# Optimization experiments

Hardware: AMD Instinct MI355X
Metric: run time of the kernel (lower is better)

## Reference

```python
import jax, jax.numpy as jnp
import numpy as np
import math

B, S, D = 1, 2048, 512
H = 8
DH = D // H
WIN = 128  # window_size
EPS = 1e-5


def _layernorm(x, g, b):
    mu = jnp.mean(x, axis=-1, keepdims=True)
    var = jnp.mean((x - mu) ** 2, axis=-1, keepdims=True)
    return (x - mu) * jax.lax.rsqrt(var + EPS) * g + b


def _local_attention(q, k, v, window_size):
    # q,k,v: [B,H,S,DH]. Faithful to F.pad + unfold: zero-padded keys
    # participate in softmax with score 0 (no masking), as in the original.
    w = window_size // 2
    W = 2 * w + 1
    kp = jnp.pad(k, ((0, 0), (0, 0), (w, w), (0, 0)))
    vp = jnp.pad(v, ((0, 0), (0, 0), (w, w), (0, 0)))
    idx = jnp.arange(q.shape[2])[:, None] + jnp.arange(W)[None, :]  # [S,W]
    k_win = kp[:, :, idx]  # [B,H,S,W,DH]
    v_win = vp[:, :, idx]  # [B,H,S,W,DH]
    scores = jnp.einsum('bhsd,bhswd->bhsw', q, k_win) / math.sqrt(q.shape[-1])
    attn = jax.nn.softmax(scores, axis=-1)
    return jnp.einsum('bhsw,bhswd->bhsd', attn, v_win)


def setup_inputs() -> dict:
    key = jax.random.key(0)
    ks = jax.random.split(key, 8)
    sc = 0.02
    return {
        'x': jax.random.normal(ks[0], (B, S, D), dtype=jnp.float32),
        'w_qkv': jax.random.normal(ks[1], (D, 3 * D), dtype=jnp.float32) * sc,
        'b_qkv': jnp.zeros((3 * D,), dtype=jnp.float32),
        'w_out': jax.random.normal(ks[2], (D, D), dtype=jnp.float32) * sc,
        'b_out': jnp.zeros((D,), dtype=jnp.float32),
        'ln_g': jnp.ones((D,), dtype=jnp.float32),
        'ln_b': jnp.zeros((D,), dtype=jnp.float32),
        'w1': jax.random.normal(ks[3], (D, 4 * D), dtype=jnp.float32) * sc,
        'b1': jnp.zeros((4 * D,), dtype=jnp.float32),
        'w2': jax.random.normal(ks[4], (4 * D, D), dtype=jnp.float32) * sc,
        'b2': jnp.zeros((D,), dtype=jnp.float32),
    }


def reference(x, w_qkv, b_qkv, w_out, b_out, ln_g, ln_b, w1, b1, w2, b2):
    residual = x
    xn = _layernorm(x, ln_g, ln_b)
    qkv = xn @ w_qkv + b_qkv                       # [B,S,3D]
    qkv = qkv.reshape(B, S, 3, H, DH)
    qkv = jnp.transpose(qkv, (2, 0, 3, 1, 4))      # [3,B,H,S,DH]
    q, k, v = qkv[0], qkv[1], qkv[2]
    attn_out = _local_attention(q, k, v, WIN)       # [B,H,S,DH]
    attn_out = jnp.transpose(attn_out, (0, 2, 1, 3)).reshape(B, S, D)
    attn_out = attn_out @ w_out + b_out
    out = residual + attn_out
    # FFN applied directly to `out` (no second norm in original)
    ffn = jax.nn.gelu(out @ w1 + b1, approximate=False) @ w2 + b2
    return out + ffn
```

## Files before the change

### kernel.cpp

```cpp
#include <hip/hip_runtime.h>
#include <math.h>

#define S_LEN 2048
#define DMODEL 512
#define NHEAD 8
#define DHEAD 64
#define LN_EPS 1e-5f

typedef __bf16 bf16;
typedef __bf16 bf16x8 __attribute__((ext_vector_type(8)));
typedef __bf16 bf16x2 __attribute__((ext_vector_type(2)));
typedef float f32x4 __attribute__((ext_vector_type(4)));

__device__ __forceinline__ float wave_reduce_sum(float x) {
#pragma unroll
  for (int off = 32; off > 0; off >>= 1) x += __shfl_xor(x, off);
  return x;
}

__global__ __launch_bounds__(256) void ln_kernel(const float* __restrict__ x,
                                                 const float* __restrict__ g,
                                                 const float* __restrict__ b,
                                                 bf16* __restrict__ xn) {
  const int row = blockIdx.x;
  const int tid = threadIdx.x;
  const float2 v = ((const float2*)(x + (size_t)row * DMODEL))[tid];
  float s = v.x + v.y;
  float s2 = v.x * v.x + v.y * v.y;
  s = wave_reduce_sum(s);
  s2 = wave_reduce_sum(s2);
  __shared__ float red[2][4];
  const int wv = tid >> 6, ln = tid & 63;
  if (ln == 0) { red[0][wv] = s; red[1][wv] = s2; }
  __syncthreads();
  s = red[0][0] + red[0][1] + red[0][2] + red[0][3];
  s2 = red[1][0] + red[1][1] + red[1][2] + red[1][3];
  const float mu = s * (1.0f / DMODEL);
  const float var = s2 * (1.0f / DMODEL) - mu * mu;
  const float rs = rsqrtf(var + LN_EPS);
  const float2 gg = ((const float2*)g)[tid];
  const float2 bb = ((const float2*)b)[tid];
  bf16x2 o;
  o[0] = (bf16)((v.x - mu) * rs * gg.x + bb.x);
  o[1] = (bf16)((v.y - mu) * rs * gg.y + bb.y);
  ((bf16x2*)(xn + (size_t)row * DMODEL))[tid] = o;
}

__global__ __launch_bounds__(256) void transpose_all(
    const float* __restrict__ w_qkv, const float* __restrict__ w_out,
    const float* __restrict__ w1, const float* __restrict__ w2,
    bf16* __restrict__ wqkvT, bf16* __restrict__ woutT,
    bf16* __restrict__ w1T, bf16* __restrict__ w2T) {
  int b = blockIdx.x;
  const float* W; bf16* WT; int K, N, bx, by;
  if (b < 768)       { W = w_qkv; WT = wqkvT; K = 512;  N = 1536; bx = b % 48; by = b / 48; }
  else if (b < 1024) { b -= 768;  W = w_out; WT = woutT; K = 512;  N = 512;  bx = b % 16; by = b / 16; }
  else if (b < 2048) { b -= 1024; W = w1;    WT = w1T;   K = 512;  N = 2048; bx = b % 64; by = b / 64; }
  else               { b -= 2048; W = w2;    WT = w2T;   K = 2048; N = 512;  bx = b % 16; by = b / 16; }
  __shared__ float t[32][33];
  const int c = threadIdx.x & 31, r8 = threadIdx.x >> 5;
  const int n0 = bx * 32, k0 = by * 32;
#pragma unroll
  for (int it = 0; it < 4; it++) {
    const int r = r8 + it * 8;
    t[r][c] = W[(size_t)(k0 + r) * N + n0 + c];
  }
  __syncthreads();
#pragma unroll
  for (int it = 0; it < 4; it++) {
    const int r = r8 + it * 8;
    WT[(size_t)(n0 + r) * K + k0 + c] = (bf16)t[c][r];
  }
}

__global__ __launch_bounds__(256) void v_transpose(const bf16* __restrict__ qkvb,
                                                   bf16* __restrict__ vT) {
  __shared__ bf16 t[32][33];
  const int c = threadIdx.x & 31, r8 = threadIdx.x >> 5;
  const int c0 = blockIdx.x * 32;
  const int s0 = blockIdx.y * 32;
#pragma unroll
  for (int it = 0; it < 4; it++) {
    const int r = r8 + it * 8;
    t[r][c] = qkvb[(size_t)(s0 + r) * 1536 + 1024 + c0 + c];
  }
  __syncthreads();
#pragma unroll
  for (int it = 0; it < 4; it++) {
    const int r = r8 + it * 8;
    vT[(size_t)(c0 + r) * S_LEN + s0 + c] = t[c][r];
  }
}

template <int MODE>
__device__ __forceinline__ void epilogue_store(float v, const float* res,
                                               float* Cf, bf16* Cb,
                                               size_t row, size_t col, int N) {
  if (MODE == 2) v = 0.5f * v * (1.0f + erff(v * 0.70710678118654752f));
  if (MODE == 1 || MODE == 3) v += res[row * N + col];
  if (MODE == 1 || MODE == 3) Cf[row * N + col] = v;
  if (MODE == 0 || MODE == 1 || MODE == 2) Cb[row * N + col] = (bf16)v;
}

template <int MODE>
__global__ __launch_bounds__(256) void mmA_kernel(const bf16* __restrict__ A,
                                                  const bf16* __restrict__ BT,
                                                  const float* __restrict__ bias,
                                                  const float* __restrict__ res,
                                                  float* __restrict__ Cf,
                                                  bf16* __restrict__ Cb,
                                                  int N, int K) {
  __shared__ bf16 As[2][64 * 64];
  __shared__ bf16 Bs[2][128 * 64];
  const int tid = threadIdx.x;
  const int wave = tid >> 6, lane = tid & 63;
  const int lr = lane & 15, kg = lane >> 4;
  const int rowBase = blockIdx.y * 64, colBase = blockIdx.x * 128;

  f32x4 acc[4][2] = {};
  const int niter = K >> 6;

  auto stage = [&](int kk, int buf) {
#pragma unroll
    for (int r = 0; r < 2; ++r) {
      const int c = wave * 2 + r;
      const int elem = c * 512 + lane * 8;
      const int s = elem >> 11, row = (elem >> 5) & 63, kp = elem & 31;
      const bf16* ga = A + (size_t)(rowBase + row) * K + kk + s * 32 + kp;
      __builtin_amdgcn_global_load_lds(
          (const __attribute__((address_space(1))) void*)ga,
          (__attribute__((address_space(3))) void*)(&As[buf][c * 512]), 16, 0, 0);
    }
#pragma unroll
    for (int r = 0; r < 4; ++r) {
      const int c = wave * 4 + r;
      const int elem = c * 512 + lane * 8;
      const int s = elem >> 12, row = (elem >> 5) & 127, kp = elem & 31;
      const bf16* gb = BT + (size_t)(colBase + row) * K + kk + s * 32 + kp;
      __builtin_amdgcn_global_load_lds(
          (const __attribute__((address_space(1))) void*)gb,
          (__attribute__((address_space(3))) void*)(&Bs[buf][c * 512]), 16, 0, 0);
    }
  };

  stage(0, 0);
  for (int it = 0; it < niter; ++it) {
    const int cur = it & 1;
    __syncthreads();
    if (it + 1 < niter) stage((it + 1) << 6, cur ^ 1);
    const bf16* as = As[cur];
    const bf16* bs = Bs[cur];
#pragma unroll
    for (int s = 0; s < 2; ++s) {
      bf16x8 af[4], bfr[2];
#pragma unroll
      for (int i = 0; i < 4; ++i)
        af[i] = *(const bf16x8*)(as + s * 2048 + (i * 16 + lr) * 32 + kg * 8);
#pragma unroll
      for (int j = 0; j < 2; ++j)
        bfr[j] = *(const bf16x8*)(bs + s * 4096 + (wave * 32 + j * 16 + lr) * 32 + kg * 8);
#pragma unroll
      for (int i = 0; i < 4; ++i)
#pragma unroll
        for (int j = 0; j < 2; ++j)
          acc[i][j] = __builtin_amdgcn_mfma_f32_16x16x32_bf16(af[i], bfr[j],
                                                              acc[i][j], 0, 0, 0);
    }
  }

#pragma unroll
  for (int j = 0; j < 2; ++j) {
    const int col = colBase + wave * 32 + j * 16 + lr;
    const float bs = bias[col];
#pragma unroll
    for (int i = 0; i < 4; ++i)
#pragma unroll
      for (int r = 0; r < 4; ++r)
        epilogue_store<MODE>(acc[i][j][r] + bs, res, Cf, Cb,
                             (size_t)(rowBase + i * 16 + kg * 4 + r),
                             (size_t)col, N);
  }
}

template <int MODE>
__global__ __launch_bounds__(256) void mmB_kernel(const bf16* __restrict__ A,
                                                  const bf16* __restrict__ BT,
                                                  const float* __restrict__ bias,
                                                  const float* __restrict__ res,
                                                  float* __restrict__ Cf,
                                                  bf16* __restrict__ Cb,
                                                  int N, int K) {
  __shared__ bf16 As[2][32 * 64];
  __shared__ bf16 Bs[2][64 * 64];
  const int tid = threadIdx.x;
  const int wave = tid >> 6, lane = tid & 63;
  const int lr = lane & 15, kg = lane >> 4;
  const int rowBase = blockIdx.y * 32, colBase = blockIdx.x * 64;

  f32x4 acc[2] = {};
  const int niter = K >> 6;

  auto stage = [&](int kk, int buf) {
    {
      const int c = wave;
      const int elem = c * 512 + lane * 8;
      const int s = elem >> 10, row = (elem >> 5) & 31, kp = elem & 31;
      const bf16* ga = A + (size_t)(rowBase + row) * K + kk + s * 32 + kp;
      __builtin_amdgcn_global_load_lds(
          (const __attribute__((address_space(1))) void*)ga,
          (__attribute__((address_space(3))) void*)(&As[buf][c * 512]), 16, 0, 0);
    }
#pragma unroll
    for (int r = 0; r < 2; ++r) {
      const int c = wave * 2 + r;
      const int elem = c * 512 + lane * 8;
      const int s = elem >> 11, row = (elem >> 5) & 63, kp = elem & 31;
      const bf16* gb = BT + (size_t)(colBase + row) * K + kk + s * 32 + kp;
      __builtin_amdgcn_global_load_lds(
          (const __attribute__((address_space(1))) void*)gb,
          (__attribute__((address_space(3))) void*)(&Bs[buf][c * 512]), 16, 0, 0);
    }
  };

  stage(0, 0);
  for (int it = 0; it < niter; ++it) {
    const int cur = it & 1;
    __syncthreads();
    if (it + 1 < niter) stage((it + 1) << 6, cur ^ 1);
    const bf16* as = As[cur];
    const bf16* bs = Bs[cur];
#pragma unroll
    for (int s = 0; s < 2; ++s) {
      bf16x8 af[2], bfr;
#pragma unroll
      for (int i = 0; i < 2; ++i)
        af[i] = *(const bf16x8*)(as + s * 1024 + (i * 16 + lr) * 32 + kg * 8);
      bfr = *(const bf16x8*)(bs + s * 2048 + (wave * 16 + lr) * 32 + kg * 8);
#pragma unroll
      for (int i = 0; i < 2; ++i)
        acc[i] = __builtin_amdgcn_mfma_f32_16x16x32_bf16(af[i], bfr, acc[i], 0, 0, 0);
    }
  }

  {
    const int col = colBase + wave * 16 + lr;
    const float bs = bias[col];
#pragma unroll
    for (int i = 0; i < 2; ++i)
#pragma unroll
      for (int r = 0; r < 4; ++r)
        epilogue_store<MODE>(acc[i][r] + bs, res, Cf, Cb,
                             (size_t)(rowBase + i * 16 + kg * 4 + r),
                             (size_t)col, N);
  }
}

__global__ __launch_bounds__(256) void attn_fused(const bf16* __restrict__ qkvb,
                                                  const bf16* __restrict__ vT,
                                                  bf16* __restrict__ attnb) {
  __shared__ bf16 Kl[192][72];
  __shared__ bf16 Vt[64][200];
  __shared__ bf16 Ql[64][72];

  const int tid = threadIdx.x;
  const int s0 = blockIdx.x * 64;
  const int hc = blockIdx.y * DHEAD;

  {
    const int row = tid >> 2, c0 = (tid & 3) * 16;
    const bf16* src = qkvb + (size_t)(s0 + row) * 1536 + hc + c0;
    *(bf16x8*)&Ql[row][c0] = *(const bf16x8*)src;
    *(bf16x8*)&Ql[row][c0 + 8] = *(const bf16x8*)(src + 8);
  }
#pragma unroll
  for (int it = 0; it < 3; it++) {
    const int row = it * 64 + (tid >> 2), c0 = (tid & 3) * 16;
    const int p = s0 - 64 + row;
    bf16x8 a, b;
    if (p >= 0 && p < S_LEN) {
      const bf16* src = qkvb + (size_t)p * 1536 + 512 + hc + c0;
      a = *(const bf16x8*)src;
      b = *(const bf16x8*)(src + 8);
    } else {
#pragma unroll
      for (int j = 0; j < 8; j++) { a[j] = (bf16)0.f; b[j] = (bf16)0.f; }
    }
    *(bf16x8*)&Kl[row][c0] = a;
    *(bf16x8*)&Kl[row][c0 + 8] = b;
  }
  {
    const int d = tid >> 2, r0 = (tid & 3) * 48;
    const bf16* src = vT + (size_t)(hc + d) * S_LEN;
#pragma unroll
    for (int i = 0; i < 6; i++) {
      const int p0 = s0 - 64 + r0 + i * 8;
      bf16x8 v;
      if (p0 >= 0 && p0 + 8 <= S_LEN) {
        v = *(const bf16x8*)(src + p0);
      } else {
#pragma unroll
        for (int j = 0; j < 8; j++) {
          const int p = p0 + j;
          v[j] = (p >= 0 && p < S_LEN) ? src[p] : (bf16)0.f;
        }
      }
      *(bf16x8*)&Vt[d][r0 + i * 8] = v;
    }
  }
  __syncthreads();

  const int wv = tid >> 6, lane = tid & 63;
  const int lr = lane & 15, kg = lane >> 4;

  f32x4 c[12] = {};
#pragma unroll
  for (int step = 0; step < 2; step++) {
    const bf16x8 qf = *(const bf16x8*)&Ql[wv * 16 + lr][step * 32 + kg * 8];
#pragma unroll
    for (int t = 0; t < 12; t++) {
      const bf16x8 kf = *(const bf16x8*)&Kl[t * 16 + lr][step * 32 + kg * 8];
      c[t] = __builtin_amdgcn_mfma_f32_16x16x32_bf16(qf, kf, c[t], 0, 0, 0);
    }
  }

  float e[12][4];
  float inv[4];
#pragma unroll
  for (int rr = 0; rr < 4; rr++) {
    const int q = wv * 16 + kg * 4 + rr;
    float m = -1e30f;
#pragma unroll
    for (int t = 0; t < 12; t++) {
      const int col = t * 16 + lr;
      if (col >= q && col <= q + 128) m = fmaxf(m, c[t][rr] * 0.125f);
    }
#pragma unroll
    for (int off = 1; off < 16; off <<= 1) m = fmaxf(m, __shfl_xor(m, off));
    float sum = 0.f;
#pragma unroll
    for (int t = 0; t < 12; t++) {
      const int col = t * 16 + lr;
      const bool valid = (col >= q) && (col <= q + 128);
      const float ev = valid ? __expf(c[t][rr] * 0.125f - m) : 0.f;
      e[t][rr] = ev;
      sum += ev;
    }
#pragma unroll
    for (int off = 1; off < 16; off <<= 1) sum += __shfl_xor(sum, off);
    inv[rr] = 1.f / sum;
  }

  __syncthreads();

  bf16* Pl = (bf16*)Kl + wv * (16 * 200);
#pragma unroll
  for (int rr = 0; rr < 4; rr++)
#pragma unroll
    for (int t = 0; t < 12; t++)
      Pl[(kg * 4 + rr) * 200 + t * 16 + lr] = (bf16)(e[t][rr] * inv[rr]);

  f32x4 o[4] = {};
#pragma unroll
  for (int step = 0; step < 6; step++) {
    const bf16x8 pf = *(const bf16x8*)&Pl[lr * 200 + step * 32 + kg * 8];
#pragma unroll
    for (int jt = 0; jt < 4; jt++) {
      const bf16x8 vf = *(const bf16x8*)&Vt[jt * 16 + lr][step * 32 + kg * 8];
      o[jt] = __builtin_amdgcn_mfma_f32_16x16x32_bf16(pf, vf, o[jt], 0, 0, 0);
    }
  }

#pragma unroll
  for (int jt = 0; jt < 4; jt++)
#pragma unroll
    for (int rr = 0; rr < 4; rr++) {
      const int q = wv * 16 + kg * 4 + rr;
      attnb[(size_t)(s0 + q) * DMODEL + hc + jt * 16 + lr] = (bf16)o[jt][rr];
    }
}

extern "C" void kernel_launch(void* const* d_in, const int* in_sizes, int n_in,
                              void* d_out, int out_size, void* d_ws, size_t ws_size,
                              hipStream_t stream) {
  const float* x     = (const float*)d_in[0];
  const float* w_qkv = (const float*)d_in[1];
  const float* b_qkv = (const float*)d_in[2];
  const float* w_out = (const float*)d_in[3];
  const float* b_out = (const float*)d_in[4];
  const float* ln_g  = (const float*)d_in[5];
  const float* ln_b  = (const float*)d_in[6];
  const float* w1    = (const float*)d_in[7];
  const float* b1    = (const float*)d_in[8];
  const float* w2    = (const float*)d_in[9];
  const float* b2    = (const float*)d_in[10];
  float* out = (float*)d_out;

  char* w = (char*)d_ws;
  const size_t MB = 1u << 20;
  bf16* xn    = (bf16*)(w + 0);
  bf16* attnb = (bf16*)(w + 0);
  bf16* qkvb  = (bf16*)(w + 2 * MB);
  bf16* outb  = (bf16*)(w + 2 * MB);
  bf16* vT    = (bf16*)(w + 8 * MB);
  bf16* h1    = (bf16*)(w + 10 * MB);
  bf16* wqkvT = (bf16*)(w + 18 * MB);
  bf16* woutT = (bf16*)(w + 19 * MB + 512 * 1024);
  bf16* w1T   = (bf16*)(w + 20 * MB);
  bf16* w2T   = (bf16*)(w + 22 * MB);

  transpose_all<<<3072, 256, 0, stream>>>(w_qkv, w_out, w1, w2,
                                          wqkvT, woutT, w1T, w2T);
  ln_kernel<<<S_LEN, 256, 0, stream>>>(x, ln_g, ln_b, xn);
  mmA_kernel<0><<<dim3(12, 32), 256, 0, stream>>>(xn, wqkvT, b_qkv, nullptr,
                                                  nullptr, qkvb, 1536, 512);
  v_transpose<<<dim3(16, 64), 256, 0, stream>>>(qkvb, vT);
  attn_fused<<<dim3(32, 8), 256, 0, stream>>>(qkvb, vT, attnb);
  mmB_kernel<1><<<dim3(8, 64), 256, 0, stream>>>(attnb, woutT, b_out, x, out,
                                                 outb, 512, 512);
  mmA_kernel<2><<<dim3(16, 32), 256, 0, stream>>>(outb, w1T, b1, nullptr,
                                                  nullptr, h1, 2048, 512);
  mmB_kernel<3><<<dim3(8, 64), 256, 0, stream>>>(h1, w2T, b2, out, out,
                                                 nullptr, 512, 2048);
}
```

Measured before the change: 147.7 us.

## Fuse LN with weight transpose, write V transposed from QKV GEMM, shrink GEMM tiles

Merges layernorm and weight transposition into a single prep launch. The QKV GEMM epilogue now writes the V columns directly in transposed layout, which removes the separate v_transpose kernel. The large GEMM tile goes from 64x128 to 64x64 with a 2x2 wave arrangement, doubling the grid for the QKV and FFN1 GEMMs. Staging addresses are precomputed outside the K loop. The aim is fewer launches and better occupancy, at the cost of less reuse per tile and strided bf16x4 stores into vT.

```diff
diff --git a/kernel.cpp b/kernel.cpp
--- a/kernel.cpp
+++ b/kernel.cpp
@@ -9,6 +9,7 @@
 
 typedef __bf16 bf16;
 typedef __bf16 bf16x8 __attribute__((ext_vector_type(8)));
+typedef __bf16 bf16x4 __attribute__((ext_vector_type(4)));
 typedef __bf16 bf16x2 __attribute__((ext_vector_type(2)));
 typedef float f32x4 __attribute__((ext_vector_type(4)));
 
@@ -18,47 +19,46 @@
   return x;
 }
 
-__global__ __launch_bounds__(256) void ln_kernel(const float* __restrict__ x,
-                                                 const float* __restrict__ g,
-                                                 const float* __restrict__ b,
-                                                 bf16* __restrict__ xn) {
-  const int row = blockIdx.x;
-  const int tid = threadIdx.x;
-  const float2 v = ((const float2*)(x + (size_t)row * DMODEL))[tid];
-  float s = v.x + v.y;
-  float s2 = v.x * v.x + v.y * v.y;
-  s = wave_reduce_sum(s);
-  s2 = wave_reduce_sum(s2);
-  __shared__ float red[2][4];
-  const int wv = tid >> 6, ln = tid & 63;
-  if (ln == 0) { red[0][wv] = s; red[1][wv] = s2; }
-  __syncthreads();
-  s = red[0][0] + red[0][1] + red[0][2] + red[0][3];
-  s2 = red[1][0] + red[1][1] + red[1][2] + red[1][3];
-  const float mu = s * (1.0f / DMODEL);
-  const float var = s2 * (1.0f / DMODEL) - mu * mu;
-  const float rs = rsqrtf(var + LN_EPS);
-  const float2 gg = ((const float2*)g)[tid];
-  const float2 bb = ((const float2*)b)[tid];
-  bf16x2 o;
-  o[0] = (bf16)((v.x - mu) * rs * gg.x + bb.x);
-  o[1] = (bf16)((v.y - mu) * rs * gg.y + bb.y);
-  ((bf16x2*)(xn + (size_t)row * DMODEL))[tid] = o;
-}
-
-__global__ __launch_bounds__(256) void transpose_all(
-    const float* __restrict__ w_qkv, const float* __restrict__ w_out,
-    const float* __restrict__ w1, const float* __restrict__ w2,
+__global__ __launch_bounds__(256) void prep_kernel(
+    const float* __restrict__ x, const float* __restrict__ ln_g,
+    const float* __restrict__ ln_b, const float* __restrict__ w_qkv,
+    const float* __restrict__ w_out, const float* __restrict__ w1,
+    const float* __restrict__ w2, bf16* __restrict__ xn,
     bf16* __restrict__ wqkvT, bf16* __restrict__ woutT,
     bf16* __restrict__ w1T, bf16* __restrict__ w2T) {
+  __shared__ float t[32][33];
   int b = blockIdx.x;
+  const int tid = threadIdx.x;
+  if (b < 2048) {
+    const float2 v = ((const float2*)(x + (size_t)b * DMODEL))[tid];
+    float s = v.x + v.y;
+    float s2 = v.x * v.x + v.y * v.y;
+    s = wave_reduce_sum(s);
+    s2 = wave_reduce_sum(s2);
+    __shared__ float red[2][4];
+    const int wv = tid >> 6, ln = tid & 63;
+    if (ln == 0) { red[0][wv] = s; red[1][wv] = s2; }
+    __syncthreads();
+    s = red[0][0] + red[0][1] + red[0][2] + red[0][3];
+    s2 = red[1][0] + red[1][1] + red[1][2] + red[1][3];
+    const float mu = s * (1.0f / DMODEL);
+    const float var = s2 * (1.0f / DMODEL) - mu * mu;
+    const float rs = rsqrtf(var + LN_EPS);
+    const float2 gg = ((const float2*)ln_g)[tid];
+    const float2 bb = ((const float2*)ln_b)[tid];
+    bf16x2 o;
+    o[0] = (bf16)((v.x - mu) * rs * gg.x + bb.x);
+    o[1] = (bf16)((v.y - mu) * rs * gg.y + bb.y);
+    ((bf16x2*)(xn + (size_t)b * DMODEL))[tid] = o;
+    return;
+  }
+  b -= 2048;
   const float* W; bf16* WT; int K, N, bx, by;
   if (b < 768)       { W = w_qkv; WT = wqkvT; K = 512;  N = 1536; bx = b % 48; by = b / 48; }
   else if (b < 1024) { b -= 768;  W = w_out; WT = woutT; K = 512;  N = 512;  bx = b % 16; by = b / 16; }
   else if (b < 2048) { b -= 1024; W = w1;    WT = w1T;   K = 512;  N = 2048; bx = b % 64; by = b / 64; }
   else               { b -= 2048; W = w2;    WT = w2T;   K = 2048; N = 512;  bx = b % 16; by = b / 16; }
-  __shared__ float t[32][33];
-  const int c = threadIdx.x & 31, r8 = threadIdx.x >> 5;
+  const int c = tid & 31, r8 = tid >> 5;
   const int n0 = bx * 32, k0 = by * 32;
 #pragma unroll
   for (int it = 0; it < 4; it++) {
@@ -70,25 +70,6 @@
   for (int it = 0; it < 4; it++) {
     const int r = r8 + it * 8;
     WT[(size_t)(n0 + r) * K + k0 + c] = (bf16)t[c][r];
-  }
-}
-
-__global__ __launch_bounds__(256) void v_transpose(const bf16* __restrict__ qkvb,
-                                                   bf16* __restrict__ vT) {
-  __shared__ bf16 t[32][33];
-  const int c = threadIdx.x & 31, r8 = threadIdx.x >> 5;
-  const int c0 = blockIdx.x * 32;
-  const int s0 = blockIdx.y * 32;
-#pragma unroll
-  for (int it = 0; it < 4; it++) {
-    const int r = r8 + it * 8;
-    t[r][c] = qkvb[(size_t)(s0 + r) * 1536 + 1024 + c0 + c];
-  }
-  __syncthreads();
-#pragma unroll
-  for (int it = 0; it < 4; it++) {
-    const int r = r8 + it * 8;
-    vT[(size_t)(c0 + r) * S_LEN + s0 + c] = t[c][r];
   }
 }
 
@@ -99,49 +80,50 @@
   if (MODE == 2) v = 0.5f * v * (1.0f + erff(v * 0.70710678118654752f));
   if (MODE == 1 || MODE == 3) v += res[row * N + col];
   if (MODE == 1 || MODE == 3) Cf[row * N + col] = v;
-  if (MODE == 0 || MODE == 1 || MODE == 2) Cb[row * N + col] = (bf16)v;
+  if (MODE == 1 || MODE == 2) Cb[row * N + col] = (bf16)v;
 }
 
 template <int MODE>
-__global__ __launch_bounds__(256) void mmA_kernel(const bf16* __restrict__ A,
+__global__ __launch_bounds__(256) void mmC_kernel(const bf16* __restrict__ A,
                                                   const bf16* __restrict__ BT,
                                                   const float* __restrict__ bias,
-                                                  const float* __restrict__ res,
-                                                  float* __restrict__ Cf,
                                                   bf16* __restrict__ Cb,
+                                                  bf16* __restrict__ vT,
                                                   int N, int K) {
   __shared__ bf16 As[2][64 * 64];
-  __shared__ bf16 Bs[2][128 * 64];
+  __shared__ bf16 Bs[2][64 * 64];
   const int tid = threadIdx.x;
   const int wave = tid >> 6, lane = tid & 63;
   const int lr = lane & 15, kg = lane >> 4;
-  const int rowBase = blockIdx.y * 64, colBase = blockIdx.x * 128;
-
-  f32x4 acc[4][2] = {};
+  const int wm = wave & 1, wn = wave >> 1;
+  const int rowBase = blockIdx.y * 64, colBase = blockIdx.x * 64;
+
+  const bf16* aP[2]; const bf16* bP[2]; int aOff[2], bOff[2];
+#pragma unroll
+  for (int r = 0; r < 2; ++r) {
+    const int c = wave * 2 + r;
+    const int elem = c * 512 + lane * 8;
+    const int s = elem >> 11, row = (elem >> 5) & 63, kp = elem & 31;
+    aP[r] = A + (size_t)(rowBase + row) * K + s * 32 + kp;
+    bP[r] = BT + (size_t)(colBase + row) * K + s * 32 + kp;
+    aOff[r] = c * 512;
+    bOff[r] = c * 512;
+  }
+
+  auto stage = [&](int kk, int buf) {
+#pragma unroll
+    for (int r = 0; r < 2; ++r) {
+      __builtin_amdgcn_global_load_lds(
+          (const __attribute__((address_space(1))) void*)(aP[r] + kk),
+          (__attribute__((address_space(3))) void*)(&As[buf][aOff[r]]), 16, 0, 0);
+      __builtin_amdgcn_global_load_lds(
+          (const __attribute__((address_space(1))) void*)(bP[r] + kk),
+          (__attribute__((address_space(3))) void*)(&Bs[buf][bOff[r]]), 16, 0, 0);
+    }
+  };
+
+  f32x4 acc[2][2] = {};
   const int niter = K >> 6;
-
-  auto stage = [&](int kk, int buf) {
-#pragma unroll
-    for (int r = 0; r < 2; ++r) {
-      const int c = wave * 2 + r;
-      const int elem = c * 512 + lane * 8;
-      const int s = elem >> 11, row = (elem >> 5) & 63, kp = elem & 31;
-      const bf16* ga = A + (size_t)(rowBase + row) * K + kk + s * 32 + kp;
-      __builtin_amdgcn_global_load_lds(
-          (const __attribute__((address_space(1))) void*)ga,
-          (__attribute__((address_space(3))) void*)(&As[buf][c * 512]), 16, 0, 0);
-    }
-#pragma unroll
-    for (int r = 0; r < 4; ++r) {
-      const int c = wave * 4 + r;
-      const int elem = c * 512 + lane * 8;
-      const int s = elem >> 12, row = (elem >> 5) & 127, kp = elem & 31;
-      const bf16* gb = BT + (size_t)(colBase + row) * K + kk + s * 32 + kp;
-      __builtin_amdgcn_global_load_lds(
-          (const __attribute__((address_space(1))) void*)gb,
-          (__attribute__((address_space(3))) void*)(&Bs[buf][c * 512]), 16, 0, 0);
-    }
-  };
 
   stage(0, 0);
   for (int it = 0; it < niter; ++it) {
@@ -152,15 +134,15 @@
     const bf16* bs = Bs[cur];
 #pragma unroll
     for (int s = 0; s < 2; ++s) {
-      bf16x8 af[4], bfr[2];
-#pragma unroll
-      for (int i = 0; i < 4; ++i)
-        af[i] = *(const bf16x8*)(as + s * 2048 + (i * 16 + lr) * 32 + kg * 8);
+      bf16x8 af[2], bfr[2];
+#pragma unroll
+      for (int i = 0; i < 2; ++i)
+        af[i] = *(const bf16x8*)(as + s * 2048 + (wm * 32 + i * 16 + lr) * 32 + kg * 8);
 #pragma unroll
       for (int j = 0; j < 2; ++j)
-        bfr[j] = *(const bf16x8*)(bs + s * 4096 + (wave * 32 + j * 16 + lr) * 32 + kg * 8);
-#pragma unroll
-      for (int i = 0; i < 4; ++i)
+        bfr[j] = *(const bf16x8*)(bs + s * 2048 + (wn * 32 + j * 16 + lr) * 32 + kg * 8);
+#pragma unroll
+      for (int i = 0; i < 2; ++i)
 #pragma unroll
         for (int j = 0; j < 2; ++j)
           acc[i][j] = __builtin_amdgcn_mfma_f32_16x16x32_bf16(af[i], bfr[j],
@@ -170,15 +152,28 @@
 
 #pragma unroll
   for (int j = 0; j < 2; ++j) {
-    const int col = colBase + wave * 32 + j * 16 + lr;
+    const int col = colBase + wn * 32 + j * 16 + lr;
     const float bs = bias[col];
-#pragma unroll
-    for (int i = 0; i < 4; ++i)
-#pragma unroll
-      for (int r = 0; r < 4; ++r)
-        epilogue_store<MODE>(acc[i][j][r] + bs, res, Cf, Cb,
-                             (size_t)(rowBase + i * 16 + kg * 4 + r),
-                             (size_t)col, N);
+    if (MODE == 4 && col >= 1024) {
+      bf16* dst = vT + (size_t)(col - 1024) * S_LEN;
+#pragma unroll
+      for (int i = 0; i < 2; ++i) {
+        bf16x4 p;
+#pragma unroll
+        for (int r = 0; r < 4; ++r) p[r] = (bf16)(acc[i][j][r] + bs);
+        *(bf16x4*)(dst + rowBase + wm * 32 + i * 16 + kg * 4) = p;
+      }
+    } else {
+#pragma unroll
+      for (int i = 0; i < 2; ++i)
+#pragma unroll
+        for (int r = 0; r < 4; ++r) {
+          const size_t row = rowBase + wm * 32 + i * 16 + kg * 4 + r;
+          float v = acc[i][j][r] + bs;
+          if (MODE == 2) v = 0.5f * v * (1.0f + erff(v * 0.70710678118654752f));
+          Cb[row * N + col] = (bf16)v;
+        }
+    }
   }
 }
 
@@ -197,30 +192,35 @@
   const int lr = lane & 15, kg = lane >> 4;
   const int rowBase = blockIdx.y * 32, colBase = blockIdx.x * 64;
 
+  const bf16* aP; const bf16* bP[2]; int aOff, bOff[2];
+  {
+    const int elem = wave * 512 + lane * 8;
+    const int s = elem >> 10, row = (elem >> 5) & 31, kp = elem & 31;
+    aP = A + (size_t)(rowBase + row) * K + s * 32 + kp;
+    aOff = wave * 512;
+  }
+#pragma unroll
+  for (int r = 0; r < 2; ++r) {
+    const int c = wave * 2 + r;
+    const int elem = c * 512 + lane * 8;
+    const int s = elem >> 11, row = (elem >> 5) & 63, kp = elem & 31;
+    bP[r] = BT + (size_t)(colBase + row) * K + s * 32 + kp;
+    bOff[r] = c * 512;
+  }
+
+  auto stage = [&](int kk, int buf) {
+    __builtin_amdgcn_global_load_lds(
+        (const __attribute__((address_space(1))) void*)(aP + kk),
+        (__attribute__((address_space(3))) void*)(&As[buf][aOff]), 16, 0, 0);
+#pragma unroll
+    for (int r = 0; r < 2; ++r)
+      __builtin_amdgcn_global_load_lds(
+          (const __attribute__((address_space(1))) void*)(bP[r] + kk),
+          (__attribute__((address_space(3))) void*)(&Bs[buf][bOff[r]]), 16, 0, 0);
+  };
+
   f32x4 acc[2] = {};
   const int niter = K >> 6;
-
-  auto stage = [&](int kk, int buf) {
-    {
-      const int c = wave;
-      const int elem = c * 512 + lane * 8;
-      const int s = elem >> 10, row = (elem >> 5) & 31, kp = elem & 31;
-      const bf16* ga = A + (size_t)(rowBase + row) * K + kk + s * 32 + kp;
-      __builtin_amdgcn_global_load_lds(
-          (const __attribute__((address_space(1))) void*)ga,
-          (__attribute__((address_space(3))) void*)(&As[buf][c * 512]), 16, 0, 0);
-    }
-#pragma unroll
-    for (int r = 0; r < 2; ++r) {
-      const int c = wave * 2 + r;
-      const int elem = c * 512 + lane * 8;
-      const int s = elem >> 11, row = (elem >> 5) & 63, kp = elem & 31;
-      const bf16* gb = BT + (size_t)(colBase + row) * K + kk + s * 32 + kp;
-      __builtin_amdgcn_global_load_lds(
-          (const __attribute__((address_space(1))) void*)gb,
-          (__attribute__((address_space(3))) void*)(&Bs[buf][c * 512]), 16, 0, 0);
-    }
-  };
 
   stage(0, 0);
   for (int it = 0; it < niter; ++it) {
@@ -408,17 +408,15 @@
   bf16* w1T   = (bf16*)(w + 20 * MB);
   bf16* w2T   = (bf16*)(w + 22 * MB);
 
-  transpose_all<<<3072, 256, 0, stream>>>(w_qkv, w_out, w1, w2,
-                                          wqkvT, woutT, w1T, w2T);
-  ln_kernel<<<S_LEN, 256, 0, stream>>>(x, ln_g, ln_b, xn);
-  mmA_kernel<0><<<dim3(12, 32), 256, 0, stream>>>(xn, wqkvT, b_qkv, nullptr,
-                                                  nullptr, qkvb, 1536, 512);
-  v_transpose<<<dim3(16, 64), 256, 0, stream>>>(qkvb, vT);
+  prep_kernel<<<5120, 256, 0, stream>>>(x, ln_g, ln_b, w_qkv, w_out, w1, w2,
+                                        xn, wqkvT, woutT, w1T, w2T);
+  mmC_kernel<4><<<dim3(24, 32), 256, 0, stream>>>(xn, wqkvT, b_qkv, qkvb, vT,
+                                                  1536, 512);
   attn_fused<<<dim3(32, 8), 256, 0, stream>>>(qkvb, vT, attnb);
   mmB_kernel<1><<<dim3(8, 64), 256, 0, stream>>>(attnb, woutT, b_out, x, out,
                                                  outb, 512, 512);
-  mmA_kernel<2><<<dim3(16, 32), 256, 0, stream>>>(outb, w1T, b1, nullptr,
-                                                  nullptr, h1, 2048, 512);
+  mmC_kernel<2><<<dim3(32, 32), 256, 0, stream>>>(outb, w1T, b1, h1, nullptr,
+                                                  2048, 512);
   mmB_kernel<3><<<dim3(8, 64), 256, 0, stream>>>(h1, w2T, b2, out, out,
                                                  nullptr, 512, 2048);
 }
```

New measurement: 141.6 us. 1.04x faster.
